# Optimization experiments

Measured on AMD Instinct MI355X. Metric: run time of the kernel, lower is better.

The kernel has to match this reference:

```python
import jax, jax.numpy as jnp
import numpy as np

NEG_INF = -9e15  # same masking constant as the torch module


def setup_inputs() -> dict:
    key = jax.random.key(0)
    k1, k2, k3 = jax.random.split(key, 3)
    B, S, F = 8, 2048, 128
    H, D = 4, 32  # n_heads, head_dim = out_features // n_heads
    features = jax.random.normal(k1, (B, S, F), dtype=jnp.float32)
    adj_matrix = jax.random.randint(k2, (B, S, S), 0, 2, dtype=jnp.int32)
    # Xavier-uniform-ish init for W [H, F, D]
    limit = float(np.sqrt(6.0 / (F + D)))
    W = jax.random.uniform(k3, (H, F, D), dtype=jnp.float32, minval=-limit, maxval=limit)
    return {"features": features, "adj_matrix": adj_matrix, "W": W}


def reference(features, adj_matrix, W):
    # features: [B, S, F], adj_matrix: [B, S, S] (>0 == edge), W: [H, F, D]
    D = W.shape[-1]
    Wh = jnp.einsum("bsf,hfd->bhsd", features, W)                 # [B, H, S, D]
    scores = jnp.einsum("bhsd,bhtd->bhst", Wh, Wh) / jnp.sqrt(jnp.float32(D))
    scores = jnp.where(adj_matrix[:, None, :, :] > 0, scores, NEG_INF)
    attn = jax.nn.softmax(scores, axis=-1)                         # [B, H, S, S]
    # dropout is identity at inference (training=False)
    h = jnp.einsum("bhst,bhtd->bhsd", attn, Wh)                    # [B, H, S, D]
    B, H, S, _ = h.shape
    # concat heads along feature dim, matching torch.cat(heads, dim=2)
    return jnp.transpose(h, (0, 2, 1, 3)).reshape(B, S, H * D)
```

## Files before the change

### kernel.cpp

```cpp
#include <hip/hip_runtime.h>
#include <hip/hip_bf16.h>
#include <stdint.h>


namespace {
constexpr int S = 2048;
constexpr int F = 128;
constexpr int H = 4;
constexpr int D = 32;

typedef __attribute__((ext_vector_type(4))) float f32x4;
typedef __attribute__((ext_vector_type(8))) short s16x8;
typedef __attribute__((ext_vector_type(4))) short s16x4;

__device__ __forceinline__ short f2bf(float f) {
  __hip_bfloat16 h = __float2bfloat16(f);
  short s; __builtin_memcpy(&s, &h, sizeof(s)); return s;
}
__device__ __forceinline__ float bf2f(short s) {
  __hip_bfloat16 h; __builtin_memcpy(&h, &s, sizeof(s));
  return __bfloat162float(h);
}
__device__ __forceinline__ unsigned pkbf(float a, float b) {
  __hip_bfloat162 h = __float22bfloat162_rn(float2{a, b});
  unsigned u; __builtin_memcpy(&u, &h, 4); return u;
}
__device__ __forceinline__ s16x8 mkfrag(uint2 a, uint2 b) {
  union { unsigned u[4]; s16x8 s; } x;
  x.u[0] = a.x; x.u[1] = a.y; x.u[2] = b.x; x.u[3] = b.y;
  return x.s;
}
__device__ __forceinline__ unsigned mk2(int x, int y) {
  return (x ? 0xFFFFu : 0u) | (y ? 0xFFFF0000u : 0u);
}

__global__ __launch_bounds__(256) void gat_proj(const float* __restrict__ feat,
                                                const float* __restrict__ W,
                                                short* __restrict__ Wh,
                                                short* __restrict__ WhT) {
  __shared__ __align__(16) short ftile[64][136];
  const int tid = threadIdx.x;
  const int w = tid >> 6;
  const int l = tid & 63;
  const int ln = l & 15, lg = l >> 4, g4 = (l >> 4) * 4;
  const int row0 = blockIdx.x * 64;
  const int b = row0 >> 11;
  const int sl0 = row0 & (S - 1);

#pragma unroll
  for (int i = 0; i < 4; ++i) {
    int c = i * 256 + tid;
    int r = c >> 4, c8 = (c & 15) * 8;
    const float* src = feat + (size_t)(row0 + r) * F + c8;
    float4 v0 = *(const float4*)src;
    float4 v1 = *(const float4*)(src + 4);
    s16x8 v;
    v[0]=f2bf(v0.x); v[1]=f2bf(v0.y); v[2]=f2bf(v0.z); v[3]=f2bf(v0.w);
    v[4]=f2bf(v1.x); v[5]=f2bf(v1.y); v[6]=f2bf(v1.z); v[7]=f2bf(v1.w);
    *(s16x8*)&ftile[r][c8] = v;
  }

  s16x8 bfr[4][2];
#pragma unroll
  for (int ks = 0; ks < 4; ++ks)
#pragma unroll
    for (int nt = 0; nt < 2; ++nt) {
      s16x8 v;
#pragma unroll
      for (int j = 0; j < 8; ++j)
        v[j] = f2bf(W[((size_t)w * F + ks*32 + lg*8 + j) * D + nt*16 + ln]);
      bfr[ks][nt] = v;
    }
  __syncthreads();

  const f32x4 z4 = {0.f, 0.f, 0.f, 0.f};
#pragma unroll
  for (int mt = 0; mt < 4; ++mt) {
    s16x8 a[4];
#pragma unroll
    for (int ks = 0; ks < 4; ++ks)
      a[ks] = *(const s16x8*)&ftile[mt*16 + ln][ks*32 + lg*8];
#pragma unroll
    for (int nt = 0; nt < 2; ++nt) {
      f32x4 c = z4;
#pragma unroll
      for (int ks = 0; ks < 4; ++ks)
        c = __builtin_amdgcn_mfma_f32_16x16x32_bf16(a[ks], bfr[ks][nt], c, 0, 0, 0);
      s16x4 tv;
#pragma unroll
      for (int r = 0; r < 4; ++r) {
        tv[r] = f2bf(c[r]);
        int srow = row0 + mt*16 + g4 + r;
        int s = srow & (S - 1);
        Wh[(((size_t)b * H + w) * S + s) * D + nt*16 + ln] = tv[r];
      }
      *(s16x4*)&WhT[(((size_t)b * H + w) * D + nt*16 + ln) * S + sl0 + mt*16 + g4] = tv;
    }
  }
}

__global__ __launch_bounds__(512) void gat_attn(const int* __restrict__ adj,
                                                const short* __restrict__ Wh,
                                                const short* __restrict__ WhT,
                                                float* __restrict__ out,
                                                float* __restrict__ PO,
                                                float* __restrict__ PS,
                                                int tiles) {
  __shared__ __align__(16) char kv[2][8192];

  const int tid = threadIdx.x;
  const int ww = tid >> 6;
  const int l = tid & 63;
  const int ln = l & 15, lg = l >> 4;

  const int N = gridDim.x;
  const int rbid = ((int)blockIdx.x & 7) * (N >> 3) + ((int)blockIdx.x >> 3);
  const int c = rbid >> 9;
  const int rem = rbid & 511;
  const int b = rem >> 6;
  const int h = (rem >> 4) & 3;
  const int qg = rem & 15;
  const int q0 = qg * 128 + ww * 16;
  const int it0 = c * tiles;

  const short* WhBH = Wh + ((size_t)b * H + h) * S * D;
  const short* WhTBH = WhT + ((size_t)b * H + h) * D * S;
  const int4* adjL = (const int4*)(adj + (size_t)b * S * S + (size_t)(q0 + ln) * S);

  const char* stgSrc;
  int stgLds;
  size_t stgStride;
  if (ww < 4) {
    stgSrc = (const char*)WhBH + ww*1024 + l*16;
    stgStride = 4096;
    int row = ww*16 + (l >> 2), db = l & 3;
    stgLds = row*64 + 16*(db ^ ((row & 3) ^ ((row >> 3) & 3)));
  } else {
    int d = (ww - 4)*8 + (l >> 3);
    stgSrc = (const char*)WhTBH + (size_t)d * S * 2 + (l & 7) * 16;
    stgStride = 128;
    stgLds = 4096 + d*128 + 16*((l & 7) ^ (d & 7));
  }

  const int kswz = (ln & 3) ^ (ln >> 2);
  int koff[4];
#pragma unroll
  for (int mt = 0; mt < 4; ++mt) {
    int lrow = 32*(mt >> 1) + 8*(ln >> 2) + 4*(mt & 1) + (ln & 3);
    koff[mt] = lrow*64 + 16*(lg ^ kswz);
  }
  int voff[2][2];
#pragma unroll
  for (int dt = 0; dt < 2; ++dt)
#pragma unroll
    for (int kt = 0; kt < 2; ++kt)
      voff[dt][kt] = 4096 + (dt*16 + ln)*128 + 16*((4*kt + lg) ^ (ln & 7));

  const float cs = 0.25503486f;
  s16x8 qf;
  {
    s16x8 v = *(const s16x8*)&WhBH[(size_t)(q0 + ln) * D + lg*8];
#pragma unroll
    for (int j = 0; j < 8; ++j) qf[j] = f2bf(bf2f(v[j]) * cs);
  }
  s16x8 onesf;
#pragma unroll
  for (int j = 0; j < 8; ++j) onesf[j] = (short)0x3F80;

  const f32x4 z4 = {0.f, 0.f, 0.f, 0.f};
  f32x4 accO[2];
  f32x4 accP = z4;
  accO[0] = z4; accO[1] = z4;

  unsigned m[8];
  {
    s16x8 stg = *(const s16x8*)(stgSrc + (size_t)it0 * stgStride);
    const int ab = it0 * 16 + 2*lg;
    int4 a0 = adjL[ab], a1 = adjL[ab + 1];
    int4 a2 = adjL[ab + 8], a3 = adjL[ab + 9];
    *(s16x8*)(&kv[0][0] + stgLds) = stg;
    m[0] = mk2(a0.x, a0.y); m[1] = mk2(a0.z, a0.w);
    m[2] = mk2(a1.x, a1.y); m[3] = mk2(a1.z, a1.w);
    m[4] = mk2(a2.x, a2.y); m[5] = mk2(a2.z, a2.w);
    m[6] = mk2(a3.x, a3.y); m[7] = mk2(a3.z, a3.w);
  }
  __syncthreads();

#pragma unroll 1
  for (int i = 0; i < tiles; ++i) {
    const int cur = i & 1, nxt = cur ^ 1;
    const int iLd = (i + 1 < tiles) ? i + 1 : i;

    s16x8 stg = *(const s16x8*)(stgSrc + (size_t)(it0 + iLd) * stgStride);
    const int ab = (it0 + iLd) * 16 + 2*lg;
    int4 a0n = adjL[ab],     a1n = adjL[ab + 1];
    int4 a2n = adjL[ab + 8], a3n = adjL[ab + 9];

    const char* kb = &kv[cur][0];
    f32x4 sv[4];
#pragma unroll
    for (int mt = 0; mt < 4; ++mt) {
      s16x8 kf = *(const s16x8*)(kb + koff[mt]);
      sv[mt] = __builtin_amdgcn_mfma_f32_16x16x32_bf16(kf, qf, z4, 0, 0, 0);
    }

    uint2 pks[4];
#pragma unroll
    for (int mt = 0; mt < 4; ++mt) {
      uint2 pk;
      pk.x = pkbf(__builtin_amdgcn_exp2f(sv[mt][0]),
                  __builtin_amdgcn_exp2f(sv[mt][1])) & m[2*mt];
      pk.y = pkbf(__builtin_amdgcn_exp2f(sv[mt][2]),
                  __builtin_amdgcn_exp2f(sv[mt][3])) & m[2*mt + 1];
      pks[mt] = pk;
    }
    s16x8 ap[2];
#pragma unroll
    for (int kt = 0; kt < 2; ++kt)
      ap[kt] = mkfrag(pks[2*kt], pks[2*kt + 1]);

#pragma unroll
    for (int dt = 0; dt < 2; ++dt)
#pragma unroll
      for (int kt = 0; kt < 2; ++kt) {
        s16x8 av = *(const s16x8*)(kb + voff[dt][kt]);
        accO[dt] = __builtin_amdgcn_mfma_f32_16x16x32_bf16(av, ap[kt], accO[dt], 0, 0, 0);
      }
#pragma unroll
    for (int kt = 0; kt < 2; ++kt)
      accP = __builtin_amdgcn_mfma_f32_16x16x32_bf16(onesf, ap[kt], accP, 0, 0, 0);

    *(s16x8*)(&kv[nxt][0] + stgLds) = stg;
    m[0] = mk2(a0n.x, a0n.y); m[1] = mk2(a0n.z, a0n.w);
    m[2] = mk2(a1n.x, a1n.y); m[3] = mk2(a1n.z, a1n.w);
    m[4] = mk2(a2n.x, a2n.y); m[5] = mk2(a2n.z, a2n.w);
    m[6] = mk2(a3n.x, a3n.y); m[7] = mk2(a3n.z, a3n.w);
    __syncthreads();
  }

  if (PO == nullptr) {
    float inv = 1.0f / accP[0];
#pragma unroll
    for (int dt = 0; dt < 2; ++dt) {
      f32x4 o;
#pragma unroll
      for (int r = 0; r < 4; ++r) o[r] = accO[dt][r] * inv;
      *(f32x4*)&out[((size_t)b * S + q0 + ln) * (H * D) + h*32 + dt*16 + 4*lg] = o;
    }
  } else {
    float* po = PO + (size_t)rbid * 4096;
#pragma unroll
    for (int dt = 0; dt < 2; ++dt)
      *(f32x4*)&po[(ww*16 + ln)*32 + dt*16 + 4*lg] = accO[dt];
    if (lg == 0) PS[(size_t)rbid * 128 + ww*16 + ln] = accP[0];
  }
}

__global__ __launch_bounds__(256) void gat_reduce(const float* __restrict__ PO,
                                                  const float* __restrict__ PS,
                                                  float* __restrict__ out,
                                                  int nchunks) {
  const int f4 = blockIdx.x * 256 + threadIdx.x;
  const int d4 = f4 & 31;
  const int h = d4 >> 3;
  const int dq = d4 & 7;
  const int s_flat = f4 >> 5;
  const int b = s_flat >> 11, s = s_flat & 2047;
  const int qg = s >> 7, ql = s & 127;

  f32x4 acc = {0.f, 0.f, 0.f, 0.f};
  float ps = 0.f;
  for (int c = 0; c < nchunks; ++c) {
    size_t base = (size_t)(c * 512 + b * 64 + h * 16 + qg);
    acc += *(const f32x4*)&PO[base * 4096 + ql*32 + dq*4];
    ps += PS[base * 128 + ql];
  }
  float inv = 1.0f / ps;
  f32x4 o = acc * inv;
  *(f32x4*)&out[(size_t)f4 * 4] = o;
}

}

extern "C" void kernel_launch(void* const* d_in, const int* in_sizes, int n_in,
                              void* d_out, int out_size, void* d_ws, size_t ws_size,
                              hipStream_t stream) {
  const float* feat = (const float*)d_in[0];
  const int* adj    = (const int*)d_in[1];
  const float* W    = (const float*)d_in[2];
  float* out        = (float*)d_out;

  short* Wh  = (short*)d_ws;
  short* WhT = Wh + (size_t)8 * H * S * D;
  const size_t whbytes = (size_t)2 * 8 * H * S * D * sizeof(short);
  const size_t chunkPO = (size_t)512 * 4096 * sizeof(float);
  const size_t chunkPS = (size_t)512 * 128 * sizeof(float);

  int nchunks = 1;
  if (ws_size >= whbytes + 2 * (chunkPO + chunkPS)) nchunks = 2;

  float* PO = nullptr;
  float* PS = nullptr;
  if (nchunks > 1) {
    PO = (float*)((char*)d_ws + whbytes);
    PS = (float*)((char*)d_ws + whbytes + (size_t)nchunks * chunkPO);
  }

  gat_proj<<<(8 * S) / 64, 256, 0, stream>>>(feat, W, Wh, WhT);
  gat_attn<<<512 * nchunks, 512, 0, stream>>>(adj, Wh, WhT, out, PO, PS, 32 / nchunks);
  if (nchunks > 1) gat_reduce<<<2048, 256, 0, stream>>>(PO, PS, out, nchunks);
}
```

Measured before the change: 85.93 us.

## Stage adjacency masks through LDS with coalesced loads; use 256-thread blocks

```diff
diff --git a/kernel.cpp b/kernel.cpp
--- a/kernel.cpp
+++ b/kernel.cpp
@@ -99,13 +99,14 @@
   }
 }
 
-__global__ __launch_bounds__(512) void gat_attn(const int* __restrict__ adj,
-                                                const short* __restrict__ Wh,
-                                                const short* __restrict__ WhT,
-                                                float* __restrict__ out,
-                                                float* __restrict__ PO,
-                                                float* __restrict__ PS,
-                                                int tiles) {
+__global__ __launch_bounds__(256, 4) void gat_attn(const int* __restrict__ adj,
+                                                   const short* __restrict__ Wh,
+                                                   const short* __restrict__ WhT,
+                                                   float* __restrict__ out,
+                                                   float* __restrict__ PO,
+                                                   float* __restrict__ PS,
+                                                   int tiles) {
+  __shared__ __align__(16) char mbuf[2][8192];
   __shared__ __align__(16) char kv[2][8192];
 
   const int tid = threadIdx.x;
@@ -115,51 +116,49 @@
 
   const int N = gridDim.x;
   const int rbid = ((int)blockIdx.x & 7) * (N >> 3) + ((int)blockIdx.x >> 3);
-  const int c = rbid >> 9;
-  const int rem = rbid & 511;
-  const int b = rem >> 6;
-  const int h = (rem >> 4) & 3;
-  const int qg = rem & 15;
-  const int q0 = qg * 128 + ww * 16;
+  const int c = rbid >> 10;
+  const int rem = rbid & 1023;
+  const int b = rem >> 7;
+  const int h = (rem >> 5) & 3;
+  const int qg = rem & 31;
+  const int qb = qg * 64;
   const int it0 = c * tiles;
 
   const short* WhBH = Wh + ((size_t)b * H + h) * S * D;
   const short* WhTBH = WhT + ((size_t)b * H + h) * D * S;
-  const int4* adjL = (const int4*)(adj + (size_t)b * S * S + (size_t)(q0 + ln) * S);
-
-  const char* stgSrc;
-  int stgLds;
-  size_t stgStride;
-  if (ww < 4) {
-    stgSrc = (const char*)WhBH + ww*1024 + l*16;
-    stgStride = 4096;
-    int row = ww*16 + (l >> 2), db = l & 3;
-    stgLds = row*64 + 16*(db ^ ((row & 3) ^ ((row >> 3) & 3)));
-  } else {
-    int d = (ww - 4)*8 + (l >> 3);
-    stgSrc = (const char*)WhTBH + (size_t)d * S * 2 + (l & 7) * 16;
-    stgStride = 128;
-    stgLds = 4096 + d*128 + 16*((l & 7) ^ (d & 7));
-  }
-
+  const int* adjB = adj + (size_t)b * S * S;
+
+  const int g4i = tid & 15, ar0 = tid >> 4;
+  const int* aSrc = adjB + (size_t)(qb + ar0) * S + 4 * g4i;
+  const short* kSrc = WhBH + (size_t)(tid >> 2) * D + (tid & 3) * 8;
+  const short* vSrc = WhTBH + (size_t)(tid >> 3) * S + (tid & 7) * 8;
+
+  const int mw0 = ar0*128 + (((g4i >> 1) ^ (ar0 & 7)) << 4) + (g4i & 1) * 8;
+  const int kwA = (tid >> 2)*64 +
+                  ((((tid & 3) ^ (((tid >> 2) & 3) ^ ((tid >> 5) & 3)))) << 4);
+  const int vwA = 4096 + (tid >> 3)*128 + ((((tid & 7) ^ ((tid >> 3) & 7))) << 4);
+
+  const int R = ww*16 + ln;
+  const int mr0 = R*128 + ((lg ^ (ln & 7)) << 4);
+  const int mr1 = R*128 + (((4 + lg) ^ (ln & 7)) << 4);
   const int kswz = (ln & 3) ^ (ln >> 2);
   int koff[4];
 #pragma unroll
   for (int mt = 0; mt < 4; ++mt) {
     int lrow = 32*(mt >> 1) + 8*(ln >> 2) + 4*(mt & 1) + (ln & 3);
-    koff[mt] = lrow*64 + 16*(lg ^ kswz);
+    koff[mt] = lrow*64 + ((lg ^ kswz) << 4);
   }
   int voff[2][2];
 #pragma unroll
   for (int dt = 0; dt < 2; ++dt)
 #pragma unroll
     for (int kt = 0; kt < 2; ++kt)
-      voff[dt][kt] = 4096 + (dt*16 + ln)*128 + 16*((4*kt + lg) ^ (ln & 7));
+      voff[dt][kt] = 4096 + (dt*16 + ln)*128 + (((4*kt + lg) ^ (ln & 7)) << 4);
 
   const float cs = 0.25503486f;
   s16x8 qf;
   {
-    s16x8 v = *(const s16x8*)&WhBH[(size_t)(q0 + ln) * D + lg*8];
+    s16x8 v = *(const s16x8*)&WhBH[(size_t)(qb + R) * D + lg*8];
 #pragma unroll
     for (int j = 0; j < 8; ++j) qf[j] = f2bf(bf2f(v[j]) * cs);
   }
@@ -172,17 +171,18 @@
   f32x4 accP = z4;
   accO[0] = z4; accO[1] = z4;
 
-  unsigned m[8];
   {
-    s16x8 stg = *(const s16x8*)(stgSrc + (size_t)it0 * stgStride);
-    const int ab = it0 * 16 + 2*lg;
-    int4 a0 = adjL[ab], a1 = adjL[ab + 1];
-    int4 a2 = adjL[ab + 8], a3 = adjL[ab + 9];
-    *(s16x8*)(&kv[0][0] + stgLds) = stg;
-    m[0] = mk2(a0.x, a0.y); m[1] = mk2(a0.z, a0.w);
-    m[2] = mk2(a1.x, a1.y); m[3] = mk2(a1.z, a1.w);
-    m[4] = mk2(a2.x, a2.y); m[5] = mk2(a2.z, a2.w);
-    m[6] = mk2(a3.x, a3.y); m[7] = mk2(a3.z, a3.w);
+    const size_t t0i = (size_t)it0 * 64;
+#pragma unroll
+    for (int j = 0; j < 4; ++j) {
+      int4 a = *(const int4*)(aSrc + (size_t)(16*j) * S + t0i);
+      *(unsigned*)(&mbuf[0][0] + mw0 + j*2048)     = mk2(a.x, a.y);
+      *(unsigned*)(&mbuf[0][0] + mw0 + j*2048 + 4) = mk2(a.z, a.w);
+    }
+    s16x8 ks = *(const s16x8*)(kSrc + t0i * D);
+    s16x8 vs = *(const s16x8*)(vSrc + t0i);
+    *(s16x8*)(&kv[0][0] + kwA) = ks;
+    *(s16x8*)(&kv[0][0] + vwA) = vs;
   }
   __syncthreads();
 
@@ -190,11 +190,17 @@
   for (int i = 0; i < tiles; ++i) {
     const int cur = i & 1, nxt = cur ^ 1;
     const int iLd = (i + 1 < tiles) ? i + 1 : i;
-
-    s16x8 stg = *(const s16x8*)(stgSrc + (size_t)(it0 + iLd) * stgStride);
-    const int ab = (it0 + iLd) * 16 + 2*lg;
-    int4 a0n = adjL[ab],     a1n = adjL[ab + 1];
-    int4 a2n = adjL[ab + 8], a3n = adjL[ab + 9];
+    const size_t tni = (size_t)(it0 + iLd) * 64;
+
+    int4 an[4];
+#pragma unroll
+    for (int j = 0; j < 4; ++j)
+      an[j] = *(const int4*)(aSrc + (size_t)(16*j) * S + tni);
+    s16x8 kstg = *(const s16x8*)(kSrc + tni * D);
+    s16x8 vstg = *(const s16x8*)(vSrc + tni);
+
+    const uint4 mA = *(const uint4*)(&mbuf[cur][0] + mr0);
+    const uint4 mB = *(const uint4*)(&mbuf[cur][0] + mr1);
 
     const char* kb = &kv[cur][0];
     f32x4 sv[4];
@@ -205,15 +211,15 @@
     }
 
     uint2 pks[4];
-#pragma unroll
-    for (int mt = 0; mt < 4; ++mt) {
-      uint2 pk;
-      pk.x = pkbf(__builtin_amdgcn_exp2f(sv[mt][0]),
-                  __builtin_amdgcn_exp2f(sv[mt][1])) & m[2*mt];
-      pk.y = pkbf(__builtin_amdgcn_exp2f(sv[mt][2]),
-                  __builtin_amdgcn_exp2f(sv[mt][3])) & m[2*mt + 1];
-      pks[mt] = pk;
-    }
+    pks[0].x = pkbf(__builtin_amdgcn_exp2f(sv[0][0]), __builtin_amdgcn_exp2f(sv[0][1])) & mA.x;
+    pks[0].y = pkbf(__builtin_amdgcn_exp2f(sv[0][2]), __builtin_amdgcn_exp2f(sv[0][3])) & mA.y;
+    pks[1].x = pkbf(__builtin_amdgcn_exp2f(sv[1][0]), __builtin_amdgcn_exp2f(sv[1][1])) & mA.z;
+    pks[1].y = pkbf(__builtin_amdgcn_exp2f(sv[1][2]), __builtin_amdgcn_exp2f(sv[1][3])) & mA.w;
+    pks[2].x = pkbf(__builtin_amdgcn_exp2f(sv[2][0]), __builtin_amdgcn_exp2f(sv[2][1])) & mB.x;
+    pks[2].y = pkbf(__builtin_amdgcn_exp2f(sv[2][2]), __builtin_amdgcn_exp2f(sv[2][3])) & mB.y;
+    pks[3].x = pkbf(__builtin_amdgcn_exp2f(sv[3][0]), __builtin_amdgcn_exp2f(sv[3][1])) & mB.z;
+    pks[3].y = pkbf(__builtin_amdgcn_exp2f(sv[3][2]), __builtin_amdgcn_exp2f(sv[3][3])) & mB.w;
+
     s16x8 ap[2];
 #pragma unroll
     for (int kt = 0; kt < 2; ++kt)
@@ -230,11 +236,13 @@
     for (int kt = 0; kt < 2; ++kt)
       accP = __builtin_amdgcn_mfma_f32_16x16x32_bf16(onesf, ap[kt], accP, 0, 0, 0);
 
-    *(s16x8*)(&kv[nxt][0] + stgLds) = stg;
-    m[0] = mk2(a0n.x, a0n.y); m[1] = mk2(a0n.z, a0n.w);
-    m[2] = mk2(a1n.x, a1n.y); m[3] = mk2(a1n.z, a1n.w);
-    m[4] = mk2(a2n.x, a2n.y); m[5] = mk2(a2n.z, a2n.w);
-    m[6] = mk2(a3n.x, a3n.y); m[7] = mk2(a3n.z, a3n.w);
+#pragma unroll
+    for (int j = 0; j < 4; ++j) {
+      *(unsigned*)(&mbuf[nxt][0] + mw0 + j*2048)     = mk2(an[j].x, an[j].y);
+      *(unsigned*)(&mbuf[nxt][0] + mw0 + j*2048 + 4) = mk2(an[j].z, an[j].w);
+    }
+    *(s16x8*)(&kv[nxt][0] + kwA) = kstg;
+    *(s16x8*)(&kv[nxt][0] + vwA) = vstg;
     __syncthreads();
   }
 
@@ -245,14 +253,14 @@
       f32x4 o;
 #pragma unroll
       for (int r = 0; r < 4; ++r) o[r] = accO[dt][r] * inv;
-      *(f32x4*)&out[((size_t)b * S + q0 + ln) * (H * D) + h*32 + dt*16 + 4*lg] = o;
+      *(f32x4*)&out[((size_t)b * S + qb + R) * (H * D) + h*32 + dt*16 + 4*lg] = o;
     }
   } else {
-    float* po = PO + (size_t)rbid * 4096;
+    float* po = PO + (size_t)rbid * 2048;
 #pragma unroll
     for (int dt = 0; dt < 2; ++dt)
-      *(f32x4*)&po[(ww*16 + ln)*32 + dt*16 + 4*lg] = accO[dt];
-    if (lg == 0) PS[(size_t)rbid * 128 + ww*16 + ln] = accP[0];
+      *(f32x4*)&po[R*32 + dt*16 + 4*lg] = accO[dt];
+    if (lg == 0) PS[(size_t)rbid * 64 + R] = accP[0];
   }
 }
 
@@ -266,14 +274,14 @@
   const int dq = d4 & 7;
   const int s_flat = f4 >> 5;
   const int b = s_flat >> 11, s = s_flat & 2047;
-  const int qg = s >> 7, ql = s & 127;
+  const int qg = s >> 6, ql = s & 63;
 
   f32x4 acc = {0.f, 0.f, 0.f, 0.f};
   float ps = 0.f;
   for (int c = 0; c < nchunks; ++c) {
-    size_t base = (size_t)(c * 512 + b * 64 + h * 16 + qg);
-    acc += *(const f32x4*)&PO[base * 4096 + ql*32 + dq*4];
-    ps += PS[base * 128 + ql];
+    size_t base = (size_t)c * 1024 + b * 128 + h * 32 + qg;
+    acc += *(const f32x4*)&PO[base * 2048 + ql*32 + dq*4];
+    ps += PS[base * 64 + ql];
   }
   float inv = 1.0f / ps;
   f32x4 o = acc * inv;
@@ -293,8 +301,8 @@
   short* Wh  = (short*)d_ws;
   short* WhT = Wh + (size_t)8 * H * S * D;
   const size_t whbytes = (size_t)2 * 8 * H * S * D * sizeof(short);
-  const size_t chunkPO = (size_t)512 * 4096 * sizeof(float);
-  const size_t chunkPS = (size_t)512 * 128 * sizeof(float);
+  const size_t chunkPO = (size_t)1024 * 2048 * sizeof(float);
+  const size_t chunkPS = (size_t)1024 * 64 * sizeof(float);
 
   int nchunks = 1;
   if (ws_size >= whbytes + 2 * (chunkPO + chunkPS)) nchunks = 2;
@@ -307,6 +315,6 @@
   }
 
   gat_proj<<<(8 * S) / 64, 256, 0, stream>>>(feat, W, Wh, WhT);
-  gat_attn<<<512 * nchunks, 512, 0, stream>>>(adj, Wh, WhT, out, PO, PS, 32 / nchunks);
+  gat_attn<<<1024 * nchunks, 256, 0, stream>>>(adj, Wh, WhT, out, PO, PS, 32 / nchunks);
   if (nchunks > 1) gat_reduce<<<2048, 256, 0, stream>>>(PO, PS, out, nchunks);
 }
```

Measured after the change: 71.31 us. 17.0% less time.
